# Performance work log

Hardware: AMD Instinct MI355X
Metric: run time of the kernel (lower is better)

## Reference

```python
import jax, jax.numpy as jnp
import numpy as np

N_NODES = 17   # fixed by Linear(256, 17) + residual add
D = 512        # feature dim
H = 8          # number of attention heads


def setup_inputs() -> dict:
    key = jax.random.key(0)
    ks = jax.random.split(key, 8)
    return {
        "Xs": jax.random.normal(ks[0], (N_NODES, D), dtype=jnp.float32),
        "ROIs_b": jax.random.uniform(ks[1], (N_NODES, 3), dtype=jnp.float32),
        "adj": jnp.zeros((N_NODES, N_NODES), dtype=jnp.float32),  # unused in forward
        "FC": jax.random.normal(ks[2], (H, D, D), dtype=jnp.float32) * (1.414 / np.sqrt(D)),
        "W1": jax.random.normal(ks[3], (H, D + 3, 256), dtype=jnp.float32) * (1.0 / np.sqrt(D + 3)),
        "b1": jnp.zeros((H, 256), dtype=jnp.float32),
        "W2": jax.random.normal(ks[4], (H, 256, N_NODES), dtype=jnp.float32) * (1.0 / np.sqrt(256)),
        "b2": jnp.zeros((H, N_NODES), dtype=jnp.float32),
        "conv_w": jax.random.normal(ks[5], (H,), dtype=jnp.float32) * 0.3,
        "conv_b": jnp.zeros((1,), dtype=jnp.float32),
    }


def reference(Xs, ROIs_b, adj, FC, W1, b1, W2, b2, conv_w, conv_b):
    # All 8 heads batched over leading axis h (original launches them as
    # separate Python-level modules).
    # f_input = relu(Xs @ FC) per head: [H, N, D]
    f = jax.nn.relu(jnp.einsum('nd,hde->hne', Xs, FC))
    # concat coordinates: [H, N, D+3]
    coords = jnp.broadcast_to(ROIs_b[None], (f.shape[0], ROIs_b.shape[0], ROIs_b.shape[1]))
    cat = jnp.concatenate([f, coords], axis=-1)
    # 2-layer MLP: Linear(515,256) -> tanh -> Linear(256,17): [H, N, 17]
    hdn = jnp.tanh(jnp.einsum('hnc,hcm->hnm', cat, W1) + b1[:, None, :])
    att = jnp.einsum('hnm,hmk->hnk', hdn, W2) + b2[:, None, :]
    # permute(1,0) then softmax over dim=1 (the N axis): [H, 17, N]
    att = jax.nn.softmax(jnp.swapaxes(att, 1, 2), axis=-1)
    # weighted sum over nodes: [H, 17, D]
    h_prime = jnp.einsum('hkn,hnd->hkd', att, f)
    # Conv1d(8,1,1) over head axis + ReLU, then residual
    out = jax.nn.relu(jnp.einsum('h,hkd->kd', conv_w, h_prime) + conv_b[0])
    Xs_out = out + Xs  # [17, 512]
    # original returns a list of per-landmark views [1,512,1,1,1]; we return
    # the equivalent stacked array plus passthrough ROIs
    return Xs_out, ROIs_b
```

## Files before the change

### kernel.cpp

```cpp
#include <hip/hip_runtime.h>

#define NN 17
#define D  512
#define H  8
#define C1 515
#define M  256

#define XPAD 20
#define RSN  36
#define RSG  (NN * RSN)
#define SMEM_FL (32 * RSG)

__device__ __forceinline__ void fma4(float4& a, float x, const float4& w) {
    a.x = fmaf(x, w.x, a.x); a.y = fmaf(x, w.y, a.y);
    a.z = fmaf(x, w.z, a.z); a.w = fmaf(x, w.w, a.w);
}

__global__ __launch_bounds__(256) void k1_f(const float* __restrict__ Xs,
                                            const float* __restrict__ FC,
                                            float* __restrict__ f) {
    const int b = blockIdx.x;
    const int et = b & 15, h = b >> 4;
    const int t = threadIdx.x, tw = t & 7, cg = t >> 3;
    __shared__ float sm[SMEM_FL];
    for (int i = t; i < NN * D; i += 256) {
        const int n = i >> 9, d = i & 511;
        sm[d * XPAD + n] = Xs[i];
    }
    __syncthreads();
    float4 acc[NN];
#pragma unroll
    for (int n = 0; n < NN; ++n) acc[n] = make_float4(0.f, 0.f, 0.f, 0.f);
    const float4* fc4 = (const float4*)(FC + (size_t)h * D * D) + et * 8 + tw;
#pragma unroll 4
    for (int i = 0; i < 16; ++i) {
        const int d = cg + (i << 5);
        const float4 w = fc4[d << 7];
        const float* xr = sm + d * XPAD;
#pragma unroll
        for (int n4 = 0; n4 < 4; ++n4) {
            const float4 x = *(const float4*)(xr + (n4 << 2));
            fma4(acc[n4 * 4 + 0], x.x, w);
            fma4(acc[n4 * 4 + 1], x.y, w);
            fma4(acc[n4 * 4 + 2], x.z, w);
            fma4(acc[n4 * 4 + 3], x.w, w);
        }
        fma4(acc[16], xr[16], w);
    }
    __syncthreads();
    float* rr = sm + cg * RSG + tw * 4;
#pragma unroll
    for (int n = 0; n < NN; ++n) *(float4*)(rr + n * RSN) = acc[n];
    __syncthreads();
    for (int i = t; i < NN * 32; i += 256) {
        const int n = i >> 5, e = i & 31;
        float s = 0.f;
#pragma unroll 8
        for (int g = 0; g < 32; ++g) s += sm[g * RSG + n * RSN + e];
        f[((h * NN + n) << 9) + (et << 5) + e] = fmaxf(s, 0.f);
    }
}

__global__ __launch_bounds__(256) void k2_hdn(const float* __restrict__ f,
                                              const float* __restrict__ ROIs,
                                              const float* __restrict__ W1,
                                              const float* __restrict__ b1,
                                              float* __restrict__ hdn) {
    const int b = blockIdx.x;
    const int mt = b & 7, h = b >> 3;
    const int t = threadIdx.x, tw = t & 7, cg = t >> 3;
    __shared__ float sm[SMEM_FL];
    for (int i = t; i < NN * D; i += 256) {
        const int n = i >> 9, d = i & 511;
        sm[d * XPAD + n] = f[((size_t)(h * NN) << 9) + i];
    }
    if (t < NN * 3) {
        const int n = t / 3, cc = t % 3;
        sm[(D + cc) * XPAD + n] = ROIs[t];
    }
    __syncthreads();
    float4 acc[NN];
#pragma unroll
    for (int n = 0; n < NN; ++n) acc[n] = make_float4(0.f, 0.f, 0.f, 0.f);
    const float4* w4 = (const float4*)(W1 + (size_t)h * C1 * M) + mt * 8 + tw;
#pragma unroll 4
    for (int i = 0; i < 16; ++i) {
        const int c = cg + (i << 5);
        const float4 w = w4[c << 6];
        const float* xr = sm + c * XPAD;
#pragma unroll
        for (int n4 = 0; n4 < 4; ++n4) {
            const float4 x = *(const float4*)(xr + (n4 << 2));
            fma4(acc[n4 * 4 + 0], x.x, w);
            fma4(acc[n4 * 4 + 1], x.y, w);
            fma4(acc[n4 * 4 + 2], x.z, w);
            fma4(acc[n4 * 4 + 3], x.w, w);
        }
        fma4(acc[16], xr[16], w);
    }
    if (cg < 3) {
        const int c = D + cg;
        const float4 w = w4[c << 6];
        const float* xr = sm + c * XPAD;
#pragma unroll
        for (int n4 = 0; n4 < 4; ++n4) {
            const float4 x = *(const float4*)(xr + (n4 << 2));
            fma4(acc[n4 * 4 + 0], x.x, w);
            fma4(acc[n4 * 4 + 1], x.y, w);
            fma4(acc[n4 * 4 + 2], x.z, w);
            fma4(acc[n4 * 4 + 3], x.w, w);
        }
        fma4(acc[16], xr[16], w);
    }
    __syncthreads();
    float* rr = sm + cg * RSG + tw * 4;
#pragma unroll
    for (int n = 0; n < NN; ++n) *(float4*)(rr + n * RSN) = acc[n];
    __syncthreads();
    for (int i = t; i < NN * 32; i += 256) {
        const int n = i >> 5, m = i & 31;
        float s = b1[h * M + (mt << 5) + m];
#pragma unroll 8
        for (int g = 0; g < 32; ++g) s += sm[g * RSG + n * RSN + m];
        hdn[(h * NN + n) * M + (mt << 5) + m] = tanhf(s);
    }
}

__global__ void k3_att(const float* __restrict__ hdn, const float* __restrict__ W2,
                       const float* __restrict__ b2, float* __restrict__ att) {
    const int h = blockIdx.x, t = threadIdx.x;
    __shared__ float sh[NN * M];
    __shared__ float swt[NN * M];
    __shared__ float sa[NN * NN];
    for (int i = t; i < NN * M; i += 320) sh[i] = hdn[h * NN * M + i];
    for (int i = t; i < NN * M; i += 320) {
        const int m = i / NN, k = i % NN;
        swt[k * M + m] = W2[(size_t)h * M * NN + i];
    }
    __syncthreads();
    if (t < NN * NN) {
        const int n = t / NN, k = t % NN;
        float acc = b2[h * NN + k];
        const float* a = sh + n * M;
        const float* w = swt + k * M;
#pragma unroll 8
        for (int m = 0; m < M; m += 4) {
            const float4 av = *(const float4*)(a + m);
            const float4 wv = *(const float4*)(w + m);
            acc = fmaf(av.x, wv.x, acc); acc = fmaf(av.y, wv.y, acc);
            acc = fmaf(av.z, wv.z, acc); acc = fmaf(av.w, wv.w, acc);
        }
        sa[k * NN + n] = acc;
    }
    __syncthreads();
    if (t < NN) {
        const int k = t;
        float mx = -1e30f;
        for (int n = 0; n < NN; ++n) mx = fmaxf(mx, sa[k * NN + n]);
        float e[NN];
        float s = 0.f;
        for (int n = 0; n < NN; ++n) { e[n] = __expf(sa[k * NN + n] - mx); s += e[n]; }
        const float inv = 1.f / s;
        for (int n = 0; n < NN; ++n) att[(h * NN + k) * NN + n] = e[n] * inv;
    }
}

__global__ void k4_out(const float* __restrict__ f, const float* __restrict__ att,
                       const float* __restrict__ conv_w, const float* __restrict__ conv_b,
                       const float* __restrict__ Xs, const float* __restrict__ ROIs,
                       float* __restrict__ out) {
    const int b = blockIdx.x;
    const int k = b >> 2, dt = b & 3;
    const int t = threadIdx.x;
    const int d = dt * 128 + t;
    __shared__ float sa[H * NN];
    __shared__ float cw[H];
    for (int i = t; i < H * NN; i += 128) {
        const int h = i / NN, n = i % NN;
        sa[i] = att[(h * NN + k) * NN + n];
    }
    if (t < H) cw[t] = conv_w[t];
    __syncthreads();
    float acc = 0.f;
#pragma unroll
    for (int h = 0; h < H; ++h) {
        float wsum = 0.f;
#pragma unroll
        for (int n = 0; n < NN; ++n)
            wsum = fmaf(sa[h * NN + n], f[(size_t)(h * NN + n) * D + d], wsum);
        acc = fmaf(cw[h], wsum, acc);
    }
    out[k * D + d] = fmaxf(acc + conv_b[0], 0.f) + Xs[k * D + d];
    if (k == 0 && dt == 0 && t < NN * 3) out[NN * D + t] = ROIs[t];
}

extern "C" void kernel_launch(void* const* d_in, const int* in_sizes, int n_in,
                              void* d_out, int out_size, void* d_ws, size_t ws_size,
                              hipStream_t stream) {
    const float* Xs     = (const float*)d_in[0];
    const float* ROIs   = (const float*)d_in[1];
    const float* FC     = (const float*)d_in[3];
    const float* W1     = (const float*)d_in[4];
    const float* b1     = (const float*)d_in[5];
    const float* W2     = (const float*)d_in[6];
    const float* b2     = (const float*)d_in[7];
    const float* conv_w = (const float*)d_in[8];
    const float* conv_b = (const float*)d_in[9];
    float* out = (float*)d_out;

    float* f   = (float*)d_ws;
    float* hdn = f + H * NN * D;
    float* att = hdn + H * NN * M;

    k1_f  <<<H * 16, 256, 0, stream>>>(Xs, FC, f);
    k2_hdn<<<H * 8,  256, 0, stream>>>(f, ROIs, W1, b1, hdn);
    k3_att<<<H,      320, 0, stream>>>(hdn, W2, b2, att);
    k4_out<<<NN * 4, 128, 0, stream>>>(f, att, conv_w, conv_b, Xs, ROIs, out);
}
```

Measured before the change: 116.9 us.

## Fuse attention-logit/softmax kernel with weighted-sum output kernel per landmark

```diff
diff --git a/kernel.cpp b/kernel.cpp
--- a/kernel.cpp
+++ b/kernel.cpp
@@ -126,72 +126,70 @@
     }
 }
 
-__global__ void k3_att(const float* __restrict__ hdn, const float* __restrict__ W2,
-                       const float* __restrict__ b2, float* __restrict__ att) {
-    const int h = blockIdx.x, t = threadIdx.x;
-    __shared__ float sh[NN * M];
-    __shared__ float swt[NN * M];
-    __shared__ float sa[NN * NN];
-    for (int i = t; i < NN * M; i += 320) sh[i] = hdn[h * NN * M + i];
-    for (int i = t; i < NN * M; i += 320) {
-        const int m = i / NN, k = i % NN;
-        swt[k * M + m] = W2[(size_t)h * M * NN + i];
-    }
-    __syncthreads();
-    if (t < NN * NN) {
-        const int n = t / NN, k = t % NN;
+__global__ __launch_bounds__(256) void k34(const float* __restrict__ hdn,
+                                           const float* __restrict__ W2,
+                                           const float* __restrict__ b2,
+                                           const float* __restrict__ f,
+                                           const float* __restrict__ conv_w,
+                                           const float* __restrict__ conv_b,
+                                           const float* __restrict__ Xs,
+                                           const float* __restrict__ ROIs,
+                                           float* __restrict__ out) {
+    const int k = blockIdx.x, t = threadIdx.x;
+    __shared__ float swk[H][M + 4];
+    __shared__ float sa[H][NN];
+    __shared__ float cw[H];
+    for (int i = t; i < H * M; i += 256) {
+        const int h = i >> 8, m = i & 255;
+        swk[h][m] = W2[(size_t)(h * M + m) * NN + k];
+    }
+    if (t < H) cw[t] = conv_w[t];
+    __syncthreads();
+    if (t < H * NN) {
+        const int h = t / NN, n = t % NN;
+        const float4* a4 = (const float4*)(hdn + (h * NN + n) * M);
+        const float4* w4 = (const float4*)(&swk[h][0]);
         float acc = b2[h * NN + k];
-        const float* a = sh + n * M;
-        const float* w = swt + k * M;
 #pragma unroll 8
-        for (int m = 0; m < M; m += 4) {
-            const float4 av = *(const float4*)(a + m);
-            const float4 wv = *(const float4*)(w + m);
+        for (int m4 = 0; m4 < M / 4; ++m4) {
+            const float4 av = a4[m4];
+            const float4 wv = w4[m4];
             acc = fmaf(av.x, wv.x, acc); acc = fmaf(av.y, wv.y, acc);
             acc = fmaf(av.z, wv.z, acc); acc = fmaf(av.w, wv.w, acc);
         }
-        sa[k * NN + n] = acc;
-    }
-    __syncthreads();
-    if (t < NN) {
-        const int k = t;
+        sa[h][n] = acc;
+    }
+    __syncthreads();
+    if (t < H) {
         float mx = -1e30f;
-        for (int n = 0; n < NN; ++n) mx = fmaxf(mx, sa[k * NN + n]);
+#pragma unroll
+        for (int n = 0; n < NN; ++n) mx = fmaxf(mx, sa[t][n]);
         float e[NN];
         float s = 0.f;
-        for (int n = 0; n < NN; ++n) { e[n] = __expf(sa[k * NN + n] - mx); s += e[n]; }
+#pragma unroll
+        for (int n = 0; n < NN; ++n) { e[n] = __expf(sa[t][n] - mx); s += e[n]; }
         const float inv = 1.f / s;
-        for (int n = 0; n < NN; ++n) att[(h * NN + k) * NN + n] = e[n] * inv;
-    }
-}
-
-__global__ void k4_out(const float* __restrict__ f, const float* __restrict__ att,
-                       const float* __restrict__ conv_w, const float* __restrict__ conv_b,
-                       const float* __restrict__ Xs, const float* __restrict__ ROIs,
-                       float* __restrict__ out) {
-    const int b = blockIdx.x;
-    const int k = b >> 2, dt = b & 3;
-    const int t = threadIdx.x;
-    const int d = dt * 128 + t;
-    __shared__ float sa[H * NN];
-    __shared__ float cw[H];
-    for (int i = t; i < H * NN; i += 128) {
-        const int h = i / NN, n = i % NN;
-        sa[i] = att[(h * NN + k) * NN + n];
-    }
-    if (t < H) cw[t] = conv_w[t];
-    __syncthreads();
-    float acc = 0.f;
-#pragma unroll
+#pragma unroll
+        for (int n = 0; n < NN; ++n) sa[t][n] = e[n] * inv;
+    }
+    __syncthreads();
+    const float cb = conv_b[0];
+    float acc0 = 0.f, acc1 = 0.f;
     for (int h = 0; h < H; ++h) {
-        float wsum = 0.f;
-#pragma unroll
-        for (int n = 0; n < NN; ++n)
-            wsum = fmaf(sa[h * NN + n], f[(size_t)(h * NN + n) * D + d], wsum);
-        acc = fmaf(cw[h], wsum, acc);
-    }
-    out[k * D + d] = fmaxf(acc + conv_b[0], 0.f) + Xs[k * D + d];
-    if (k == 0 && dt == 0 && t < NN * 3) out[NN * D + t] = ROIs[t];
+        float w0 = 0.f, w1 = 0.f;
+#pragma unroll
+        for (int n = 0; n < NN; ++n) {
+            const float a = sa[h][n];
+            const float* fr = f + (size_t)((h * NN + n) << 9);
+            w0 = fmaf(a, fr[t], w0);
+            w1 = fmaf(a, fr[t + 256], w1);
+        }
+        acc0 = fmaf(cw[h], w0, acc0);
+        acc1 = fmaf(cw[h], w1, acc1);
+    }
+    out[(k << 9) + t]       = fmaxf(acc0 + cb, 0.f) + Xs[(k << 9) + t];
+    out[(k << 9) + t + 256] = fmaxf(acc1 + cb, 0.f) + Xs[(k << 9) + t + 256];
+    if (k == 0 && t < NN * 3) out[NN * D + t] = ROIs[t];
 }
 
 extern "C" void kernel_launch(void* const* d_in, const int* in_sizes, int n_in,
@@ -210,10 +208,8 @@
 
     float* f   = (float*)d_ws;
     float* hdn = f + H * NN * D;
-    float* att = hdn + H * NN * M;
 
     k1_f  <<<H * 16, 256, 0, stream>>>(Xs, FC, f);
     k2_hdn<<<H * 8,  256, 0, stream>>>(f, ROIs, W1, b1, hdn);
-    k3_att<<<H,      320, 0, stream>>>(hdn, W2, b2, att);
-    k4_out<<<NN * 4, 128, 0, stream>>>(f, att, conv_w, conv_b, Xs, ROIs, out);
-}
+    k34   <<<NN,     256, 0, stream>>>(hdn, W2, b2, f, conv_w, conv_b, Xs, ROIs, out);
+}
```

After: 107.3 us. -8.2%, faster.
